# Performance work log

Measured on AMD Instinct MI355X. Metric: run time of the kernel, lower is better.

## Reference

```python
import jax, jax.numpy as jnp
import numpy as np

LOG2 = float(np.log(2.0))

def ssp(x):
    # ShiftedSoftplus: softplus(x) - log(2)
    return jax.nn.softplus(x) - LOG2

B, N, F, R, P = 8, 1000, 128, 20, 512000  # batch, atoms, n_atom_basis=n_filters, n_rbf, n_pairs

def setup_inputs() -> dict:
    key = jax.random.key(0)
    ks = jax.random.split(key, 14)
    inv = lambda d: 1.0 / np.sqrt(d)
    return {
        "x": jax.random.normal(ks[0], (B, N, F), dtype=jnp.float32),
        "f_ij": jax.random.normal(ks[1], (P, R), dtype=jnp.float32),
        "idx_i": jax.random.randint(ks[2], (P,), 0, B * N, dtype=jnp.int32),
        "idx_j": jax.random.randint(ks[3], (P,), 0, B * N, dtype=jnp.int32),
        "rcut_ij": jax.random.uniform(ks[4], (P,), dtype=jnp.float32),
        # input_to_feature: Linear(F, F)
        "W_in": jax.random.normal(ks[5], (F, F), dtype=jnp.float32) * inv(F),
        "b_in": jnp.zeros((F,), dtype=jnp.float32),
        # filter_network: Linear(R, F) -> SSP -> Linear(F, F)
        "Wf1": jax.random.normal(ks[6], (R, F), dtype=jnp.float32) * inv(R),
        "bf1": jnp.zeros((F,), dtype=jnp.float32),
        "Wf2": jax.random.normal(ks[7], (F, F), dtype=jnp.float32) * inv(F),
        "bf2": jnp.zeros((F,), dtype=jnp.float32),
        # feature_to_output: Linear(F, F) -> SSP -> Linear(F, F)
        "Wo1": jax.random.normal(ks[8], (F, F), dtype=jnp.float32) * inv(F),
        "bo1": jnp.zeros((F,), dtype=jnp.float32),
        "Wo2": jax.random.normal(ks[9], (F, F), dtype=jnp.float32) * inv(F),
        "bo2": jnp.zeros((F,), dtype=jnp.float32),
    }

def reference(x, f_ij, idx_i, idx_j, rcut_ij,
              W_in, b_in, Wf1, bf1, Wf2, bf2, Wo1, bo1, Wo2, bo2):
    batch, n_atoms = x.shape[0], x.shape[1]
    # input_to_feature
    h = (x @ W_in + b_in).reshape(batch * n_atoms, -1)      # [B*N, F]
    # filter network on radial basis, modulated by cutoff
    Wij = ssp(f_ij @ Wf1 + bf1) @ Wf2 + bf2                 # [P, F]
    Wij = Wij * rcut_ij[:, None]
    # gather neighbor features, elementwise filter, scatter-add to center atom
    x_ij = h[idx_j] * Wij                                   # [P, F]
    agg = jax.ops.segment_sum(x_ij, idx_i, num_segments=batch * n_atoms)  # [B*N, F]
    # feature_to_output
    out = ssp(agg @ Wo1 + bo1) @ Wo2 + bo2
    return out.reshape(batch, n_atoms, 128)
```

## Files before the change

### kernel.cpp

```cpp
#include <hip/hip_runtime.h>
#include <math.h>

#define FDIM 128
#define RDIM 20
#define BN   8000
#define NPAIR 512000
#define PB   64

typedef __attribute__((ext_vector_type(8))) short short8v;
typedef __attribute__((ext_vector_type(4))) float float4v;

__device__ __forceinline__ float sspf_fast(float x) {
    return fmaxf(x, 0.0f) + __logf(1.0f + __expf(-fabsf(x))) - 0.69314718055994531f;
}
__device__ __forceinline__ float sspf(float x) {
    return fmaxf(x, 0.0f) + log1pf(expf(-fabsf(x))) - 0.69314718055994531f;
}

__device__ __forceinline__ unsigned short f2bf(float x) {
    union { float f; unsigned u; } v; v.f = x;
    unsigned r = (v.u + 0x7FFFu + ((v.u >> 16) & 1u)) >> 16;
    return (unsigned short)r;
}

__global__ __launch_bounds__(256) void hist_kernel(
    const int* __restrict__ idx_i, int* __restrict__ cnt)
{
    const int p = blockIdx.x * 256 + threadIdx.x;
    if (p < NPAIR) atomicAdd(&cnt[idx_i[p]], 1);
}

__global__ __launch_bounds__(1024) void scan_kernel(
    const int* __restrict__ cnt, int* __restrict__ cursor)
{
    __shared__ int part[1024];
    const int t = threadIdx.x;
    int v[8]; int sum = 0;
    #pragma unroll
    for (int k = 0; k < 8; ++k) {
        const int i = t * 8 + k;
        const int c = (i < BN) ? cnt[i] : 0;
        v[k] = sum; sum += c;
    }
    part[t] = sum;
    __syncthreads();
    for (int off = 1; off < 1024; off <<= 1) {
        const int x = (t >= off) ? part[t - off] : 0;
        __syncthreads();
        part[t] += x;
        __syncthreads();
    }
    const int base = (t == 0) ? 0 : part[t - 1];
    #pragma unroll
    for (int k = 0; k < 8; ++k) {
        const int i = t * 8 + k;
        if (i < BN) cursor[i] = base + v[k];
    }
}

__global__ __launch_bounds__(256) void scatter_kernel(
    const int* __restrict__ idx_i, int* __restrict__ cursor, int* __restrict__ perm)
{
    const int p = blockIdx.x * 256 + threadIdx.x;
    if (p < NPAIR) {
        const int pos = atomicAdd(&cursor[idx_i[p]], 1);
        perm[pos] = p;
    }
}

template<bool SSP>
__global__ __launch_bounds__(256) void rowgemm_kernel(
    const float* __restrict__ A, const float* __restrict__ W,
    const float* __restrict__ bias, float* __restrict__ C)
{
    __shared__ float rowlds[16 * 128];
    const int tid = threadIdx.x;
    const int blk = blockIdx.x;
    for (int s = tid; s < 16 * 128; s += 256)
        rowlds[s] = A[blk * 16 * 128 + s];
    __syncthreads();

    const int lane = tid & 63;
    const int wave = tid >> 6;
    const float b0 = bias[lane];
    const float b1 = bias[64 + lane];
    float acc[4][2];
    #pragma unroll
    for (int rr = 0; rr < 4; ++rr) { acc[rr][0] = b0; acc[rr][1] = b1; }

    #pragma unroll 4
    for (int m = 0; m < 128; ++m) {
        const float w0 = W[m * 128 + lane];
        const float w1 = W[m * 128 + 64 + lane];
        #pragma unroll
        for (int rr = 0; rr < 4; ++rr) {
            const float av = rowlds[(wave * 4 + rr) * 128 + m];
            acc[rr][0] = fmaf(av, w0, acc[rr][0]);
            acc[rr][1] = fmaf(av, w1, acc[rr][1]);
        }
    }

    #pragma unroll
    for (int rr = 0; rr < 4; ++rr) {
        const int p = blk * 16 + wave * 4 + rr;
        float v0 = acc[rr][0], v1 = acc[rr][1];
        if (SSP) { v0 = sspf(v0); v1 = sspf(v1); }
        C[p * 128 + lane]      = v0;
        C[p * 128 + 64 + lane] = v1;
    }
}

__global__ __launch_bounds__(256) void pairs_mfma_agg(
    const float* __restrict__ f_ij, const int* __restrict__ idx_i,
    const int* __restrict__ idx_j, const float* __restrict__ rcut,
    const float* __restrict__ Wf1, const float* __restrict__ bf1,
    const float* __restrict__ Wf2, const float* __restrict__ bf2,
    const float* __restrict__ h, const int* __restrict__ rowEnd,
    const int* __restrict__ perm, float* __restrict__ agg)
{
    __shared__ unsigned short xt[64 * 128];
    __shared__ int   rrs[PB];
    __shared__ int   jjs[PB];
    __shared__ float rcs[PB];

    const int tid = threadIdx.x;
    const int w   = tid >> 6;
    const int l   = tid & 63;
    const int l15 = l & 15;
    const int l4  = l >> 4;
    const int swz = (l15 & 7) << 4;

    const int row0 = blockIdx.x * 16;
    const int s0 = (row0 == 0) ? 0 : rowEnd[row0 - 1];
    const int s1 = rowEnd[row0 + 15];

    short8v wf1a[2];
    #pragma unroll
    for (int kt2 = 0; kt2 < 2; ++kt2) {
        const int ck = w * 32 + kt2 * 16 + l15;
        #pragma unroll
        for (int e = 0; e < 8; ++e) {
            const int r = l4 * 8 + e;
            const float val = (r < RDIM) ? Wf1[r * 128 + ck] : 0.0f;
            wf1a[kt2][e] = (short)f2bf(val);
        }
    }
    short8v wf2a[2][4];
    #pragma unroll
    for (int mt = 0; mt < 2; ++mt) {
        const int c = w * 32 + mt * 16 + l15;
        #pragma unroll
        for (int ks = 0; ks < 4; ++ks) {
            #pragma unroll
            for (int e = 0; e < 8; ++e) {
                const int k = ks * 32 + l4 * 8 + e;
                wf2a[mt][ks][e] = (short)f2bf(Wf2[k * 128 + c]);
            }
        }
    }
    float b1v[2][4], b2v[2][4];
    #pragma unroll
    for (int t = 0; t < 2; ++t)
        #pragma unroll
        for (int j = 0; j < 4; ++j) {
            b1v[t][j] = bf1[w * 32 + t * 16 + l4 * 4 + j];
            b2v[t][j] = bf2[w * 32 + t * 16 + l4 * 4 + j];
        }

    float4v accD[2];
    accD[0] = float4v{0.f, 0.f, 0.f, 0.f};
    accD[1] = float4v{0.f, 0.f, 0.f, 0.f};

    for (int s = s0; s < s1; s += PB) {
        __syncthreads();

        if (tid < PB) {
            const int q  = s + tid;
            const int qc = q < s1 ? q : s1 - 1;
            const int pid = perm[qc];
            rrs[tid] = idx_i[pid] - row0;
            jjs[tid] = idx_j[pid];
            rcs[tid] = (q < s1) ? rcut[pid] : 0.0f;
        }

        short8v ffr[4];
        #pragma unroll
        for (int nt = 0; nt < 4; ++nt) {
            const int q = s + nt * 16 + l15;
            const int pid = perm[q < s1 ? q : s1 - 1];
            const float* fb = &f_ij[(size_t)pid * RDIM];
            float4 fa = {0.f, 0.f, 0.f, 0.f}, fc = {0.f, 0.f, 0.f, 0.f};
            if (l4 < 3) fa = *(const float4*)(fb + l4 * 8);
            if (l4 < 2) fc = *(const float4*)(fb + l4 * 8 + 4);
            ffr[nt][0] = (short)f2bf(fa.x); ffr[nt][1] = (short)f2bf(fa.y);
            ffr[nt][2] = (short)f2bf(fa.z); ffr[nt][3] = (short)f2bf(fa.w);
            ffr[nt][4] = (short)f2bf(fc.x); ffr[nt][5] = (short)f2bf(fc.y);
            ffr[nt][6] = (short)f2bf(fc.z); ffr[nt][7] = (short)f2bf(fc.w);
        }
        __syncthreads();

        float4 hv[4][2];
        #pragma unroll
        for (int nt = 0; nt < 4; ++nt) {
            const int gj = jjs[nt * 16 + l15] * 128;
            hv[nt][0] = *(const float4*)&h[gj + w * 32 + l4 * 4];
            hv[nt][1] = *(const float4*)&h[gj + w * 32 + 16 + l4 * 4];
        }

        #pragma unroll
        for (int kt2 = 0; kt2 < 2; ++kt2) {
            #pragma unroll
            for (int nt = 0; nt < 4; ++nt) {
                float4v acc1 = {0.f, 0.f, 0.f, 0.f};
                acc1 = __builtin_amdgcn_mfma_f32_16x16x32_bf16(wf1a[kt2], ffr[nt], acc1, 0, 0, 0);
                unsigned short pk[4];
                #pragma unroll
                for (int j = 0; j < 4; ++j)
                    pk[j] = f2bf(sspf_fast(acc1[j] + b1v[kt2][j]));
                const int row = nt * 16 + l15;
                const int byte = row * 256 + ((w * 64 + kt2 * 32 + l4 * 8) ^ swz);
                *(unsigned long long*)((char*)xt + byte) =
                    (unsigned long long)pk[0] | ((unsigned long long)pk[1] << 16) |
                    ((unsigned long long)pk[2] << 32) | ((unsigned long long)pk[3] << 48);
            }
        }
        __syncthreads();

        float4v a2[2][4];
        #pragma unroll
        for (int mt = 0; mt < 2; ++mt)
            #pragma unroll
            for (int nt = 0; nt < 4; ++nt)
                a2[mt][nt] = float4v{0.f, 0.f, 0.f, 0.f};

        #pragma unroll
        for (int ks = 0; ks < 4; ++ks) {
            short8v bfr[4];
            #pragma unroll
            for (int nt = 0; nt < 4; ++nt) {
                const int row = nt * 16 + l15;
                const int byte = row * 256 + ((ks * 64 + l4 * 16) ^ swz);
                bfr[nt] = *(const short8v*)((const char*)xt + byte);
            }
            #pragma unroll
            for (int mt = 0; mt < 2; ++mt)
                #pragma unroll
                for (int nt = 0; nt < 4; ++nt)
                    a2[mt][nt] = __builtin_amdgcn_mfma_f32_16x16x32_bf16(
                        wf2a[mt][ks], bfr[nt], a2[mt][nt], 0, 0, 0);
        }
        __syncthreads();

        #pragma unroll
        for (int nt = 0; nt < 4; ++nt) {
            const int p = nt * 16 + l15;
            const float r = rcs[p];
            #pragma unroll
            for (int mt = 0; mt < 2; ++mt) {
                #pragma unroll
                for (int j = 0; j < 4; ++j) {
                    const int c = w * 32 + mt * 16 + l4 * 4 + j;
                    const float xv = hv[nt][mt][j] * ((a2[mt][nt][j] + b2v[mt][j]) * r);
                    const int byte = c * 128 + ((p * 2) ^ ((c & 7) << 4));
                    *(unsigned short*)((char*)xt + byte) = f2bf(xv);
                }
            }
        }
        __syncthreads();

        #pragma unroll
        for (int ks = 0; ks < 2; ++ks) {
            short8v sfr;
            #pragma unroll
            for (int e = 0; e < 8; ++e) {
                const int pr = ks * 32 + l4 * 8 + e;
                sfr[e] = (rrs[pr] == l15) ? (short)0x3F80 : (short)0;
            }
            #pragma unroll
            for (int mt = 0; mt < 2; ++mt) {
                const int c = w * 32 + mt * 16 + l15;
                const int byte = c * 128 + ((ks * 64 + l4 * 16) ^ swz);
                const short8v xfr = *(const short8v*)((const char*)xt + byte);
                accD[mt] = __builtin_amdgcn_mfma_f32_16x16x32_bf16(xfr, sfr, accD[mt], 0, 0, 0);
            }
        }
    }

    #pragma unroll
    for (int mt = 0; mt < 2; ++mt) {
        float4 v;
        v.x = accD[mt][0]; v.y = accD[mt][1]; v.z = accD[mt][2]; v.w = accD[mt][3];
        *(float4*)&agg[(size_t)(row0 + l15) * 128 + w * 32 + mt * 16 + l4 * 4] = v;
    }
}

extern "C" void kernel_launch(void* const* d_in, const int* in_sizes, int n_in,
                              void* d_out, int out_size, void* d_ws, size_t ws_size,
                              hipStream_t stream) {
    const float* x     = (const float*)d_in[0];
    const float* f_ij  = (const float*)d_in[1];
    const int*   idx_i = (const int*)  d_in[2];
    const int*   idx_j = (const int*)  d_in[3];
    const float* rcut  = (const float*)d_in[4];
    const float* W_in  = (const float*)d_in[5];
    const float* b_in  = (const float*)d_in[6];
    const float* Wf1   = (const float*)d_in[7];
    const float* bf1   = (const float*)d_in[8];
    const float* Wf2   = (const float*)d_in[9];
    const float* bf2   = (const float*)d_in[10];
    const float* Wo1   = (const float*)d_in[11];
    const float* bo1   = (const float*)d_in[12];
    const float* Wo2   = (const float*)d_in[13];
    const float* bo2   = (const float*)d_in[14];
    float* out = (float*)d_out;

    const size_t SLAB = (size_t)BN * FDIM * sizeof(float);
    float* h   = (float*)d_ws;
    float* t1  = (float*)((char*)d_ws + SLAB);
    float* agg = (float*)((char*)d_ws + 2 * SLAB);
    int* perm   = (int*)t1;
    int* cnt    = (int*)((char*)t1 + (size_t)NPAIR * 4);
    int* cursor = cnt + 8001;

    hipMemsetAsync(cnt, 0, (BN + 1) * sizeof(int), stream);
    hist_kernel<<<NPAIR / 256, 256, 0, stream>>>(idx_i, cnt);
    scan_kernel<<<1, 1024, 0, stream>>>(cnt, cursor);
    scatter_kernel<<<NPAIR / 256, 256, 0, stream>>>(idx_i, cursor, perm);

    rowgemm_kernel<false><<<BN / 16, 256, 0, stream>>>(x, W_in, b_in, h);

    pairs_mfma_agg<<<BN / 16, 256, 0, stream>>>(
        f_ij, idx_i, idx_j, rcut, Wf1, bf1, Wf2, bf2, h, cursor, perm, agg);

    rowgemm_kernel<true><<<BN / 16, 256, 0, stream>>>(agg, Wo1, bo1, t1);
    rowgemm_kernel<false><<<BN / 16, 256, 0, stream>>>(t1, Wo2, bo2, out);
}
```

Measured before the change: 231.8 us.

## Software-pipeline pair loads, store h in bf16, halve rows per block

```diff
diff --git a/kernel.cpp b/kernel.cpp
--- a/kernel.cpp
+++ b/kernel.cpp
@@ -6,6 +6,7 @@
 #define BN   8000
 #define NPAIR 512000
 #define PB   64
+#define ROWS 8
 
 typedef __attribute__((ext_vector_type(8))) short short8v;
 typedef __attribute__((ext_vector_type(4))) float float4v;
@@ -68,10 +69,10 @@
     }
 }
 
-template<bool SSP>
+template<bool SSP, bool BF16OUT>
 __global__ __launch_bounds__(256) void rowgemm_kernel(
     const float* __restrict__ A, const float* __restrict__ W,
-    const float* __restrict__ bias, float* __restrict__ C)
+    const float* __restrict__ bias, void* __restrict__ Cv)
 {
     __shared__ float rowlds[16 * 128];
     const int tid = threadIdx.x;
@@ -105,23 +106,31 @@
         const int p = blk * 16 + wave * 4 + rr;
         float v0 = acc[rr][0], v1 = acc[rr][1];
         if (SSP) { v0 = sspf(v0); v1 = sspf(v1); }
-        C[p * 128 + lane]      = v0;
-        C[p * 128 + 64 + lane] = v1;
-    }
-}
-
-__global__ __launch_bounds__(256) void pairs_mfma_agg(
+        if (BF16OUT) {
+            unsigned short* C = (unsigned short*)Cv;
+            C[p * 128 + lane]      = f2bf(v0);
+            C[p * 128 + 64 + lane] = f2bf(v1);
+        } else {
+            float* C = (float*)Cv;
+            C[p * 128 + lane]      = v0;
+            C[p * 128 + 64 + lane] = v1;
+        }
+    }
+}
+
+__global__ __launch_bounds__(256) void pairs_v5(
     const float* __restrict__ f_ij, const int* __restrict__ idx_i,
     const int* __restrict__ idx_j, const float* __restrict__ rcut,
     const float* __restrict__ Wf1, const float* __restrict__ bf1,
     const float* __restrict__ Wf2, const float* __restrict__ bf2,
-    const float* __restrict__ h, const int* __restrict__ rowEnd,
+    const unsigned short* __restrict__ h2, const int* __restrict__ rowEnd,
     const int* __restrict__ perm, float* __restrict__ agg)
 {
-    __shared__ unsigned short xt[64 * 128];
-    __shared__ int   rrs[PB];
-    __shared__ int   jjs[PB];
-    __shared__ float rcs[PB];
+    __shared__ unsigned short act[64 * 128];
+    __shared__ unsigned short xbuf[64 * 128];
+    __shared__ float         rcs[2][PB];
+    __shared__ int           jjs[2][PB];
+    __shared__ unsigned char rrs8[2][PB];
 
     const int tid = threadIdx.x;
     const int w   = tid >> 6;
@@ -130,9 +139,9 @@
     const int l4  = l >> 4;
     const int swz = (l15 & 7) << 4;
 
-    const int row0 = blockIdx.x * 16;
+    const int row0 = blockIdx.x * ROWS;
     const int s0 = (row0 == 0) ? 0 : rowEnd[row0 - 1];
-    const int s1 = rowEnd[row0 + 15];
+    const int s1 = rowEnd[row0 + ROWS - 1];
 
     short8v wf1a[2];
     #pragma unroll
@@ -171,25 +180,15 @@
     accD[0] = float4v{0.f, 0.f, 0.f, 0.f};
     accD[1] = float4v{0.f, 0.f, 0.f, 0.f};
 
-    for (int s = s0; s < s1; s += PB) {
-        __syncthreads();
-
-        if (tid < PB) {
-            const int q  = s + tid;
-            const int qc = q < s1 ? q : s1 - 1;
-            const int pid = perm[qc];
-            rrs[tid] = idx_i[pid] - row0;
-            jjs[tid] = idx_j[pid];
-            rcs[tid] = (q < s1) ? rcut[pid] : 0.0f;
-        }
-
-        short8v ffr[4];
-        #pragma unroll
-        for (int nt = 0; nt < 4; ++nt) {
-            const int q = s + nt * 16 + l15;
-            const int pid = perm[q < s1 ? q : s1 - 1];
-            const float* fb = &f_ij[(size_t)pid * RDIM];
-            float4 fa = {0.f, 0.f, 0.f, 0.f}, fc = {0.f, 0.f, 0.f, 0.f};
+    short8v ffr[4];
+    float4  mreg = {0.f, 0.f, 0.f, 0.f};
+    {
+        #pragma unroll
+        for (int nt = 0; nt < 4; ++nt) {
+            int q = s0 + nt * 16 + l15; if (q > NPAIR - 1) q = NPAIR - 1;
+            const int pid = perm[q];
+            const float* fb = f_ij + (size_t)pid * RDIM;
+            float4 fa = {0.f,0.f,0.f,0.f}, fc = {0.f,0.f,0.f,0.f};
             if (l4 < 3) fa = *(const float4*)(fb + l4 * 8);
             if (l4 < 2) fc = *(const float4*)(fb + l4 * 8 + 4);
             ffr[nt][0] = (short)f2bf(fa.x); ffr[nt][1] = (short)f2bf(fa.y);
@@ -197,14 +196,22 @@
             ffr[nt][4] = (short)f2bf(fc.x); ffr[nt][5] = (short)f2bf(fc.y);
             ffr[nt][6] = (short)f2bf(fc.z); ffr[nt][7] = (short)f2bf(fc.w);
         }
-        __syncthreads();
-
-        float4 hv[4][2];
-        #pragma unroll
-        for (int nt = 0; nt < 4; ++nt) {
-            const int gj = jjs[nt * 16 + l15] * 128;
-            hv[nt][0] = *(const float4*)&h[gj + w * 32 + l4 * 4];
-            hv[nt][1] = *(const float4*)&h[gj + w * 32 + 16 + l4 * 4];
+        if (tid < PB) {
+            int q = s0 + tid; if (q > NPAIR - 1) q = NPAIR - 1;
+            const int pid = perm[q];
+            mreg.x = rcut[pid];
+            mreg.y = __int_as_float(idx_j[pid]);
+            mreg.z = __int_as_float(idx_i[pid]);
+        }
+    }
+
+    int tb = 0;
+    for (int s = s0; s < s1; s += PB, tb ^= 1) {
+        if (tid < PB) {
+            const int q = s + tid;
+            rcs[tb][tid]  = (q < s1) ? mreg.x : 0.0f;
+            jjs[tb][tid]  = __float_as_int(mreg.y);
+            rrs8[tb][tid] = (unsigned char)(__float_as_int(mreg.z) - row0);
         }
 
         #pragma unroll
@@ -219,12 +226,34 @@
                     pk[j] = f2bf(sspf_fast(acc1[j] + b1v[kt2][j]));
                 const int row = nt * 16 + l15;
                 const int byte = row * 256 + ((w * 64 + kt2 * 32 + l4 * 8) ^ swz);
-                *(unsigned long long*)((char*)xt + byte) =
+                *(unsigned long long*)((char*)act + byte) =
                     (unsigned long long)pk[0] | ((unsigned long long)pk[1] << 16) |
                     ((unsigned long long)pk[2] << 32) | ((unsigned long long)pk[3] << 48);
             }
         }
         __syncthreads();
+
+        const int sn = s + PB;
+
+        int pidn[4];
+        #pragma unroll
+        for (int nt = 0; nt < 4; ++nt) {
+            int q = sn + nt * 16 + l15; if (q > NPAIR - 1) q = NPAIR - 1;
+            pidn[nt] = perm[q];
+        }
+        int pidm = 0;
+        if (tid < PB) {
+            int q = sn + tid; if (q > NPAIR - 1) q = NPAIR - 1;
+            pidm = perm[q];
+        }
+
+        unsigned long long hvb[4][2];
+        #pragma unroll
+        for (int nt = 0; nt < 4; ++nt) {
+            const int gj = jjs[tb][nt * 16 + l15] << 7;
+            hvb[nt][0] = *(const unsigned long long*)&h2[gj + w * 32 + l4 * 4];
+            hvb[nt][1] = *(const unsigned long long*)&h2[gj + w * 32 + 16 + l4 * 4];
+        }
 
         float4v a2[2][4];
         #pragma unroll
@@ -240,7 +269,7 @@
             for (int nt = 0; nt < 4; ++nt) {
                 const int row = nt * 16 + l15;
                 const int byte = row * 256 + ((ks * 64 + l4 * 16) ^ swz);
-                bfr[nt] = *(const short8v*)((const char*)xt + byte);
+                bfr[nt] = *(const short8v*)((const char*)act + byte);
             }
             #pragma unroll
             for (int mt = 0; mt < 2; ++mt)
@@ -249,20 +278,38 @@
                     a2[mt][nt] = __builtin_amdgcn_mfma_f32_16x16x32_bf16(
                         wf2a[mt][ks], bfr[nt], a2[mt][nt], 0, 0, 0);
         }
-        __syncthreads();
+
+        #pragma unroll
+        for (int nt = 0; nt < 4; ++nt) {
+            const float* fb = f_ij + (size_t)pidn[nt] * RDIM;
+            float4 fa = {0.f,0.f,0.f,0.f}, fc = {0.f,0.f,0.f,0.f};
+            if (l4 < 3) fa = *(const float4*)(fb + l4 * 8);
+            if (l4 < 2) fc = *(const float4*)(fb + l4 * 8 + 4);
+            ffr[nt][0] = (short)f2bf(fa.x); ffr[nt][1] = (short)f2bf(fa.y);
+            ffr[nt][2] = (short)f2bf(fa.z); ffr[nt][3] = (short)f2bf(fa.w);
+            ffr[nt][4] = (short)f2bf(fc.x); ffr[nt][5] = (short)f2bf(fc.y);
+            ffr[nt][6] = (short)f2bf(fc.z); ffr[nt][7] = (short)f2bf(fc.w);
+        }
+        if (tid < PB) {
+            mreg.x = rcut[pidm];
+            mreg.y = __int_as_float(idx_j[pidm]);
+            mreg.z = __int_as_float(idx_i[pidm]);
+        }
 
         #pragma unroll
         for (int nt = 0; nt < 4; ++nt) {
             const int p = nt * 16 + l15;
-            const float r = rcs[p];
+            const float r = rcs[tb][p];
             #pragma unroll
             for (int mt = 0; mt < 2; ++mt) {
                 #pragma unroll
                 for (int j = 0; j < 4; ++j) {
                     const int c = w * 32 + mt * 16 + l4 * 4 + j;
-                    const float xv = hv[nt][mt][j] * ((a2[mt][nt][j] + b2v[mt][j]) * r);
+                    const float hf = __uint_as_float(
+                        (unsigned)((hvb[nt][mt] >> (16 * j)) & 0xFFFFULL) << 16);
+                    const float xv = hf * ((a2[mt][nt][j] + b2v[mt][j]) * r);
                     const int byte = c * 128 + ((p * 2) ^ ((c & 7) << 4));
-                    *(unsigned short*)((char*)xt + byte) = f2bf(xv);
+                    *(unsigned short*)((char*)xbuf + byte) = f2bf(xv);
                 }
             }
         }
@@ -270,27 +317,31 @@
 
         #pragma unroll
         for (int ks = 0; ks < 2; ++ks) {
+            const unsigned long long rb =
+                *(const unsigned long long*)&rrs8[tb][ks * 32 + l4 * 8];
             short8v sfr;
             #pragma unroll
             for (int e = 0; e < 8; ++e) {
-                const int pr = ks * 32 + l4 * 8 + e;
-                sfr[e] = (rrs[pr] == l15) ? (short)0x3F80 : (short)0;
+                const unsigned rv = (unsigned)((rb >> (8 * e)) & 0xFFull);
+                sfr[e] = (rv == (unsigned)l15) ? (short)0x3F80 : (short)0;
             }
             #pragma unroll
             for (int mt = 0; mt < 2; ++mt) {
                 const int c = w * 32 + mt * 16 + l15;
-                const int byte = c * 128 + ((ks * 64 + l4 * 16) ^ swz);
-                const short8v xfr = *(const short8v*)((const char*)xt + byte);
+                const int byte = c * 128 + ((ks * 64 + l4 * 16) ^ ((c & 7) << 4));
+                const short8v xfr = *(const short8v*)((const char*)xbuf + byte);
                 accD[mt] = __builtin_amdgcn_mfma_f32_16x16x32_bf16(xfr, sfr, accD[mt], 0, 0, 0);
             }
         }
     }
 
-    #pragma unroll
-    for (int mt = 0; mt < 2; ++mt) {
-        float4 v;
-        v.x = accD[mt][0]; v.y = accD[mt][1]; v.z = accD[mt][2]; v.w = accD[mt][3];
-        *(float4*)&agg[(size_t)(row0 + l15) * 128 + w * 32 + mt * 16 + l4 * 4] = v;
+    if (l15 < ROWS) {
+        #pragma unroll
+        for (int mt = 0; mt < 2; ++mt) {
+            float4 v;
+            v.x = accD[mt][0]; v.y = accD[mt][1]; v.z = accD[mt][2]; v.w = accD[mt][3];
+            *(float4*)&agg[(size_t)(row0 + l15) * 128 + w * 32 + mt * 16 + l4 * 4] = v;
+        }
     }
 }
 
@@ -314,10 +365,9 @@
     const float* bo2   = (const float*)d_in[14];
     float* out = (float*)d_out;
 
-    const size_t SLAB = (size_t)BN * FDIM * sizeof(float);
-    float* h   = (float*)d_ws;
-    float* t1  = (float*)((char*)d_ws + SLAB);
-    float* agg = (float*)((char*)d_ws + 2 * SLAB);
+    unsigned short* h2 = (unsigned short*)d_ws;
+    float* agg = (float*)((char*)d_ws + 2048000);
+    float* t1  = (float*)((char*)d_ws + 2048000 + 4096000);
     int* perm   = (int*)t1;
     int* cnt    = (int*)((char*)t1 + (size_t)NPAIR * 4);
     int* cursor = cnt + 8001;
@@ -327,11 +377,11 @@
     scan_kernel<<<1, 1024, 0, stream>>>(cnt, cursor);
     scatter_kernel<<<NPAIR / 256, 256, 0, stream>>>(idx_i, cursor, perm);
 
-    rowgemm_kernel<false><<<BN / 16, 256, 0, stream>>>(x, W_in, b_in, h);
-
-    pairs_mfma_agg<<<BN / 16, 256, 0, stream>>>(
-        f_ij, idx_i, idx_j, rcut, Wf1, bf1, Wf2, bf2, h, cursor, perm, agg);
-
-    rowgemm_kernel<true><<<BN / 16, 256, 0, stream>>>(agg, Wo1, bo1, t1);
-    rowgemm_kernel<false><<<BN / 16, 256, 0, stream>>>(t1, Wo2, bo2, out);
-}
+    rowgemm_kernel<false, true><<<BN / 16, 256, 0, stream>>>(x, W_in, b_in, h2);
+
+    pairs_v5<<<BN / ROWS, 256, 0, stream>>>(
+        f_ij, idx_i, idx_j, rcut, Wf1, bf1, Wf2, bf2, h2, cursor, perm, agg);
+
+    rowgemm_kernel<true,  false><<<BN / 16, 256, 0, stream>>>(agg, Wo1, bo1, t1);
+    rowgemm_kernel<false, false><<<BN / 16, 256, 0, stream>>>(t1, Wo2, bo2, out);
+}
```

New measurement: 274.4 us. 18.4% more time.
